# Kernel tuning notes

Measured on AMD Instinct MI355X. Metric: run time of the kernel, lower is better.

## Reference

```python
import jax, jax.numpy as jnp
import numpy as np

B, S, D = 2, 2048, 768
H, DK, DV = 12, 64, 64


def setup_inputs() -> dict:
    key = jax.random.key(0)
    ks = jax.random.split(key, 12)
    sc = 0.02
    return {
        'q': jax.random.normal(ks[0], (B, S, D), jnp.float32),
        'k': jax.random.normal(ks[1], (B, S, D), jnp.float32),
        'v': jax.random.normal(ks[2], (B, S, D), jnp.float32),
        'mask': jnp.zeros((B, H, S, S), jnp.float32),
        'Wq': jax.random.normal(ks[3], (D, H * DK), jnp.float32) * sc,
        'bq': jnp.zeros((H * DK,), jnp.float32),
        'Wk': jax.random.normal(ks[4], (D, H * DK), jnp.float32) * sc,
        'bk': jnp.zeros((H * DK,), jnp.float32),
        'Wv': jax.random.normal(ks[5], (D, H * DV), jnp.float32) * sc,
        'bv': jnp.zeros((H * DV,), jnp.float32),
        'Wo': jax.random.normal(ks[6], (H * DV, D), jnp.float32) * sc,
        'bo': jnp.zeros((D,), jnp.float32),
    }


def reference(q, k, v, mask, Wq, bq, Wk, bk, Wv, bv, Wo, bo):
    b, s, _ = q.shape
    # projections -> [B, H, S, Dk/Dv]
    Q = (q @ Wq + bq).reshape(b, s, H, DK).transpose(0, 2, 1, 3)
    K = (k @ Wk + bk).reshape(b, s, H, DK).transpose(0, 2, 1, 3)
    V = (v @ Wv + bv).reshape(b, s, H, DV).transpose(0, 2, 1, 3)
    scale = 1.0 / np.sqrt(DK).astype(np.float32)
    scores = jnp.einsum('bhqd,bhkd->bhqk', Q, K) * scale + mask
    attn = jax.nn.softmax(scores, axis=-1)  # dropout rate 0.0 -> identity
    ctx = jnp.einsum('bhqk,bhkd->bhqd', attn, V)
    ctx = ctx.transpose(0, 2, 1, 3).reshape(b, s, H * DV)
    out = ctx @ Wo + bo
    return out, attn
```

## Files before the change

### kernel.cpp

```cpp
#include <hip/hip_runtime.h>
#include <hip/hip_bf16.h>

typedef unsigned short u16;
typedef __attribute__((ext_vector_type(8))) short s16x8;
typedef __attribute__((ext_vector_type(4))) float f32x4;

#define MFMA16(a, b, c) __builtin_amdgcn_mfma_f32_16x16x32_bf16((a), (b), (c), 0, 0, 0)

__device__ __forceinline__ float b2f(u16 u) {
    union { float f; unsigned int i; } c; c.i = ((unsigned int)u) << 16; return c.f;
}
__device__ __forceinline__ u16 f2b(float f) {
    union { float f; unsigned int i; } c; c.f = f;
    unsigned int i = c.i;
    return (u16)((i + 0x7fffu + ((i >> 16) & 1u)) >> 16);
}

__device__ __forceinline__ s16x8 load8b(const void* base, size_t idx, int isf32) {
    if (!isf32) {
        return *(const s16x8*)((const u16*)base + idx);
    } else {
        const float* p = (const float*)base + idx;
        f32x4 a = *(const f32x4*)p;
        f32x4 b = *(const f32x4*)(p + 4);
        s16x8 v;
        v[0] = (short)f2b(a[0]); v[1] = (short)f2b(a[1]);
        v[2] = (short)f2b(a[2]); v[3] = (short)f2b(a[3]);
        v[4] = (short)f2b(b[0]); v[5] = (short)f2b(b[1]);
        v[6] = (short)f2b(b[2]); v[7] = (short)f2b(b[3]);
        return v;
    }
}
__device__ __forceinline__ float loadsc(const void* base, size_t idx, int isf32) {
    return isf32 ? ((const float*)base)[idx] : b2f(((const u16*)base)[idx]);
}
__device__ __forceinline__ float loadsc_nt(const void* base, size_t idx, int isf32) {
    if (isf32) return __builtin_nontemporal_load((const float*)base + idx);
    u16 u = __builtin_nontemporal_load((const u16*)base + idx);
    return b2f(u);
}

__global__ __launch_bounds__(64) void k_detect(const u16* __restrict__ q, int* __restrict__ flag) {
    int t = threadIdx.x;
    int cnt = 0;
#pragma unroll
    for (int i = 0; i < 16; i++) {
        u16 u = q[t * 16 + i];
        int e = (u >> 7) & 0xFF;
        cnt += (e >= 110 && e <= 135) ? 1 : 0;
    }
#pragma unroll
    for (int off = 32; off > 0; off >>= 1) cnt += __shfl_down(cnt, off);
    if (t == 0) *flag = (cnt < 850) ? 1 : 0;
}

__global__ __launch_bounds__(256) void k_transpose(
    const void* __restrict__ w0, const void* __restrict__ w1,
    const void* __restrict__ w2, const void* __restrict__ w3,
    u16* __restrict__ wt, const int* __restrict__ flag)
{
    __shared__ __align__(16) u16 T[64 * 65];
    const int isf32 = *flag;
    const int z = blockIdx.z;
    const void* W = (z == 0) ? w0 : (z == 1) ? w1 : (z == 2) ? w2 : w3;
    u16* WT = wt + (size_t)z * 589824;
    const int n0 = blockIdx.x * 64, k0 = blockIdx.y * 64;
    const int t = threadIdx.x;
    const int r = t >> 3, c = (t & 7) * 8;
    for (int rr = r; rr < 64; rr += 32) {
        s16x8 v = load8b(W, (size_t)(k0 + rr) * 768 + n0 + c, isf32);
#pragma unroll
        for (int j = 0; j < 8; j++) T[(c + j) * 65 + rr] = (u16)v[j];
    }
    __syncthreads();
    const int n = t >> 3, kc = (t & 7) * 8;
    for (int nn = n; nn < 64; nn += 32) {
        s16x8 v;
#pragma unroll
        for (int j = 0; j < 8; j++) v[j] = (short)T[nn * 65 + kc + j];
        *(s16x8*)&WT[(size_t)(n0 + nn) * 768 + k0 + kc] = v;
    }
}

__device__ __forceinline__ void gemm_body(
    const void* __restrict__ A, int a_isf32, const u16* __restrict__ WT,
    const void* __restrict__ bias, int b_isf32, void* __restrict__ out,
    int out_isf32, int epi, int head, int m0)
{
    __shared__ __align__(16) u16 As[128 * 72];
    __shared__ __align__(16) u16 Bs[64 * 72];
    const int t = threadIdx.x;
    const int lane = t & 63, wave = t >> 6;
    const int quad = lane >> 4, l16 = lane & 15;
    const int mrow_base = (wave >> 1) * 64;
    const int ncol_base = (wave & 1) * 32;
    const int hbase = head * 64;

    f32x4 acc[4][2];
#pragma unroll
    for (int mt = 0; mt < 4; mt++)
#pragma unroll
        for (int nt = 0; nt < 2; nt++) acc[mt][nt] = (f32x4){0.f, 0.f, 0.f, 0.f};

    for (int k0 = 0; k0 < 768; k0 += 64) {
#pragma unroll
        for (int i = 0; i < 4; i++) {
            int seg = t + 256 * i;
            int r = seg >> 3, c = (seg & 7) * 8;
            *(s16x8*)&As[r * 72 + c] = load8b(A, (size_t)(m0 + r) * 768 + k0 + c, a_isf32);
        }
#pragma unroll
        for (int i = 0; i < 2; i++) {
            int seg = t + 256 * i;
            int r = seg >> 3, c = (seg & 7) * 8;
            *(s16x8*)&Bs[r * 72 + c] = *(const s16x8*)&WT[(size_t)(hbase + r) * 768 + k0 + c];
        }
        __syncthreads();
#pragma unroll
        for (int ks = 0; ks < 2; ks++) {
            s16x8 af[4], bf[2];
#pragma unroll
            for (int mt = 0; mt < 4; mt++)
                af[mt] = *(const s16x8*)&As[(mrow_base + mt * 16 + l16) * 72 + ks * 32 + quad * 8];
#pragma unroll
            for (int nt = 0; nt < 2; nt++)
                bf[nt] = *(const s16x8*)&Bs[(ncol_base + nt * 16 + l16) * 72 + ks * 32 + quad * 8];
#pragma unroll
            for (int mt = 0; mt < 4; mt++)
#pragma unroll
                for (int nt = 0; nt < 2; nt++)
                    acc[mt][nt] = MFMA16(af[mt], bf[nt], acc[mt][nt]);
        }
        __syncthreads();
    }

    if (epi == 2) {
#pragma unroll
        for (int mt = 0; mt < 4; mt++)
#pragma unroll
            for (int nt = 0; nt < 2; nt++) {
                int nc = ncol_base + nt * 16 + l16;
                float bvv = loadsc(bias, hbase + nc, b_isf32);
#pragma unroll
                for (int r = 0; r < 4; r++) {
                    int m = m0 + mrow_base + mt * 16 + quad * 4 + r;
                    float val = acc[mt][nt][r] + bvv;
                    size_t idx = (size_t)m * 768 + hbase + nc;
                    if (out_isf32) ((float*)out)[idx] = val;
                    else           ((u16*)out)[idx] = f2b(val);
                }
            }
    } else if (epi == 0) {
        u16* ob = (u16*)out;
#pragma unroll
        for (int mt = 0; mt < 4; mt++)
#pragma unroll
            for (int nt = 0; nt < 2; nt++) {
                int nc = ncol_base + nt * 16 + l16;
                float bvv = loadsc(bias, hbase + nc, b_isf32);
#pragma unroll
                for (int r = 0; r < 4; r++) {
                    int m = m0 + mrow_base + mt * 16 + quad * 4 + r;
                    int bidx = m >> 11, s = m & 2047;
                    ob[(((size_t)bidx * 12 + head) * 2048 + s) * 64 + nc] =
                        f2b(acc[mt][nt][r] + bvv);
                }
            }
    } else {
        u16* ob = (u16*)out;
        u16* Ts = As;
#pragma unroll
        for (int mt = 0; mt < 4; mt++)
#pragma unroll
            for (int nt = 0; nt < 2; nt++) {
                int nc = ncol_base + nt * 16 + l16;
                float bvv = loadsc(bias, hbase + nc, b_isf32);
#pragma unroll
                for (int r = 0; r < 4; r++) {
                    int ml = mrow_base + mt * 16 + quad * 4 + r;
                    Ts[nc * 136 + ml] = f2b(acc[mt][nt][r] + bvv);
                }
            }
        __syncthreads();
        const int bidx = m0 >> 11, sbase = m0 & 2047;
#pragma unroll
        for (int i = 0; i < 4; i++) {
            int seg = t + 256 * i;
            int dv = seg >> 4, scc = (seg & 15) * 8;
            s16x8 vv = *(const s16x8*)&Ts[dv * 136 + scc];
            *(s16x8*)&ob[(((size_t)bidx * 12 + head) * 64 + dv) * 2048 + sbase + scc] = vv;
        }
    }
}

__global__ __launch_bounds__(256) void k_qkv(
    const void* __restrict__ q, const void* __restrict__ k, const void* __restrict__ v,
    const u16* __restrict__ wt,
    const void* __restrict__ bq, const void* __restrict__ bk, const void* __restrict__ bv,
    u16* __restrict__ Q, u16* __restrict__ K, u16* __restrict__ Vt,
    const int* __restrict__ flag)
{
    const int isf32 = *flag;
    const int z = blockIdx.z;
    const void* A = (z == 0) ? q : (z == 1) ? k : v;
    const u16* WTz = wt + (size_t)z * 589824;
    const void* bias = (z == 0) ? bq : (z == 1) ? bk : bv;
    u16* out = (z == 0) ? Q : (z == 1) ? K : Vt;
    gemm_body(A, isf32, WTz, bias, isf32, out, 0, (z == 2) ? 1 : 0, blockIdx.y, blockIdx.x * 128);
}

__global__ __launch_bounds__(256) void k_oproj(
    const u16* __restrict__ ctx, const u16* __restrict__ wto,
    const void* __restrict__ bo, void* __restrict__ out,
    const int* __restrict__ flag)
{
    const int isf32 = *flag;
    gemm_body(ctx, 0, wto, bo, isf32, out, isf32, 2, blockIdx.y, blockIdx.x * 128);
}

__device__ __forceinline__ int sw_off(int row, int col) {
    int unit = col >> 3;
    int slot = (unit + row) & 7;
    return row * 2048 + (((unit & ~7) | slot) << 3) + (col & 7);
}

__global__ __launch_bounds__(512, 4) void k_attn(
    const u16* __restrict__ Q, const u16* __restrict__ K,
    const u16* __restrict__ Vt, const void* __restrict__ mask,
    void* __restrict__ outbase, u16* __restrict__ ctx,
    const int* __restrict__ flag)
{
    __shared__ __align__(16) u16 sc[16 * 2048];
    __shared__ __align__(16) float part[1024];
    __shared__ float wmax[16][8];
    const int isf32 = *flag;
    const int t = threadIdx.x;
    const int lane = t & 63, wave = t >> 6;
    const int quad = lane >> 4, l16 = lane & 15;
    const int q0 = blockIdx.x * 16;
    const int h = blockIdx.y, b = blockIdx.z;
    const int bh = b * 12 + h;

    const u16* Qb = Q + ((size_t)bh * 2048 + q0) * 64;
    const s16x8 qf0 = *(const s16x8*)&Qb[l16 * 64 + quad * 8];
    const s16x8 qf1 = *(const s16x8*)&Qb[l16 * 64 + 32 + quad * 8];

    const u16* Kb = K + (size_t)bh * 2048 * 64;
    const size_t mrow0 = ((size_t)bh * 2048 + q0) * 2048;

    float rm[4] = {-3.4e38f, -3.4e38f, -3.4e38f, -3.4e38f};
#pragma unroll 4
    for (int it = 0; it < 16; it++) {
        const int kc = it * 128 + wave * 16;
        const u16* kp = &Kb[(size_t)(kc + l16) * 64 + quad * 8];
        s16x8 kf0 = *(const s16x8*)kp;
        s16x8 kf1 = *(const s16x8*)(kp + 32);
        f32x4 a = (f32x4){0.f, 0.f, 0.f, 0.f};
        a = MFMA16(qf0, kf0, a);
        a = MFMA16(qf1, kf1, a);
        const int col = kc + l16;
#pragma unroll
        for (int r = 0; r < 4; r++) {
            const int row = quad * 4 + r;
            float m = loadsc_nt(mask, mrow0 + (size_t)row * 2048 + col, isf32);
            float x = a[r] * 0.125f + m;
            sc[sw_off(row, col)] = f2b(x);
            rm[r] = fmaxf(rm[r], x);
        }
    }
#pragma unroll
    for (int off = 8; off > 0; off >>= 1)
#pragma unroll
        for (int r = 0; r < 4; r++) rm[r] = fmaxf(rm[r], __shfl_xor(rm[r], off));
    if (l16 == 0) {
#pragma unroll
        for (int r = 0; r < 4; r++) wmax[quad * 4 + r][wave] = rm[r];
    }
    __syncthreads();

    const int row = t >> 5, j32 = t & 31;
    float mx = wmax[row][0];
#pragma unroll
    for (int w = 1; w < 8; w++) mx = fmaxf(mx, wmax[row][w]);

    float sum = 0.f;
#pragma unroll 4
    for (int i = 0; i < 8; i++) {
        const int c0 = j32 * 8 + i * 256;
        s16x8* sp = (s16x8*)&sc[sw_off(row, c0)];
        s16x8 sv = *sp, nv;
#pragma unroll
        for (int j = 0; j < 8; j++) {
            float e = __expf(b2f((u16)sv[j]) - mx);
            nv[j] = (short)f2b(e);
            sum += e;
        }
        *sp = nv;
    }
#pragma unroll
    for (int off = 16; off > 0; off >>= 1) sum += __shfl_xor(sum, off);
    const float inv = 1.0f / sum;

    const size_t aoff = 3145728 + mrow0 + (size_t)row * 2048;
#pragma unroll 2
    for (int i = 0; i < 8; i++) {
        const int c0 = j32 * 8 + i * 256;
        s16x8* sp = (s16x8*)&sc[sw_off(row, c0)];
        s16x8 sv = *sp, pv;
        float p[8];
#pragma unroll
        for (int j = 0; j < 8; j++) {
            p[j] = b2f((u16)sv[j]) * inv;
            pv[j] = (short)f2b(p[j]);
        }
        *sp = pv;
        if (isf32) {
            float* arow = (float*)outbase + aoff;
            f32x4 lo = (f32x4){p[0], p[1], p[2], p[3]};
            f32x4 hi = (f32x4){p[4], p[5], p[6], p[7]};
            __builtin_nontemporal_store(lo, (f32x4*)&arow[c0]);
            __builtin_nontemporal_store(hi, (f32x4*)&arow[c0 + 4]);
        } else {
            u16* arow = (u16*)outbase + aoff;
            __builtin_nontemporal_store(pv, (s16x8*)&arow[c0]);
        }
    }
    __syncthreads();

    const int wg = wave >> 2;
    const int dv = (wave & 3) * 16 + l16;
    const u16* vrow = Vt + ((size_t)bh * 64 + dv) * 2048;
    f32x4 o = (f32x4){0.f, 0.f, 0.f, 0.f};
    const int kbase = wg * 32;
#pragma unroll 4
    for (int kk = 0; kk < 32; kk++) {
        const int kcol = (kbase + kk) * 32 + quad * 8;
        s16x8 pa = *(const s16x8*)&sc[sw_off(l16, kcol)];
        s16x8 vb = *(const s16x8*)&vrow[kcol];
        o = MFMA16(pa, vb, o);
    }
    if (wg == 1) *(f32x4*)&part[((wave & 3) * 64 + lane) * 4] = o;
    __syncthreads();
    if (wg == 0) {
        f32x4 o2 = *(const f32x4*)&part[((wave & 3) * 64 + lane) * 4];
#pragma unroll
        for (int r = 0; r < 4; r++)
            ctx[((size_t)b * 2048 + q0 + quad * 4 + r) * 768 + h * 64 + dv] =
                f2b(o[r] + o2[r]);
    }
}

extern "C" void kernel_launch(void* const* d_in, const int* in_sizes, int n_in,
                              void* d_out, int out_size, void* d_ws, size_t ws_size,
                              hipStream_t stream) {
    const void* q    = d_in[0];
    const void* k    = d_in[1];
    const void* v    = d_in[2];
    const void* mask = d_in[3];
    const void* Wq   = d_in[4];
    const void* bq   = d_in[5];
    const void* Wk   = d_in[6];
    const void* bk   = d_in[7];
    const void* Wv   = d_in[8];
    const void* bv   = d_in[9];
    const void* Wo   = d_in[10];
    const void* bo   = d_in[11];

    u16* ws  = (u16*)d_ws;
    u16* WT  = ws;
    u16* Qb  = ws + 2359296;
    u16* Kb  = ws + 5505024;
    u16* Vtb = ws + 8650752;
    u16* ctx = ws + 11796480;
    int* flag = (int*)(ws + 14942208);

    k_detect<<<1, 64, 0, stream>>>((const u16*)q, flag);
    k_transpose<<<dim3(12, 12, 4), 256, 0, stream>>>(Wq, Wk, Wv, Wo, WT, flag);
    k_qkv<<<dim3(32, 12, 3), 256, 0, stream>>>(q, k, v, WT, bq, bk, bv, Qb, Kb, Vtb, flag);
    k_attn<<<dim3(128, 12, 2), 512, 0, stream>>>(Qb, Kb, Vtb, mask, d_out, ctx, flag);
    k_oproj<<<dim3(32, 12, 1), 256, 0, stream>>>(ctx, WT + 3 * 589824, bo, d_out, flag);
}
```

Before: 1.008 ms.

## Vectorize mask loads in softmax pass and defer normalization to PV output

Result: faster. 924.3 us (-8.3%).

```diff
diff --git a/kernel.cpp b/kernel.cpp
--- a/kernel.cpp
+++ b/kernel.cpp
@@ -34,10 +34,18 @@
 __device__ __forceinline__ float loadsc(const void* base, size_t idx, int isf32) {
     return isf32 ? ((const float*)base)[idx] : b2f(((const u16*)base)[idx]);
 }
-__device__ __forceinline__ float loadsc_nt(const void* base, size_t idx, int isf32) {
-    if (isf32) return __builtin_nontemporal_load((const float*)base + idx);
-    u16 u = __builtin_nontemporal_load((const u16*)base + idx);
-    return b2f(u);
+__device__ __forceinline__ void load8f_nt(const void* base, size_t idx, int isf32, float* o) {
+    if (!isf32) {
+        s16x8 m = __builtin_nontemporal_load((const s16x8*)((const u16*)base + idx));
+#pragma unroll
+        for (int j = 0; j < 8; j++) o[j] = b2f((u16)m[j]);
+    } else {
+        const float* p = (const float*)base + idx;
+        f32x4 a = __builtin_nontemporal_load((const f32x4*)p);
+        f32x4 b = __builtin_nontemporal_load((const f32x4*)(p + 4));
+        o[0] = a[0]; o[1] = a[1]; o[2] = a[2]; o[3] = a[3];
+        o[4] = b[0]; o[5] = b[1]; o[6] = b[2]; o[7] = b[3];
+    }
 }
 
 __global__ __launch_bounds__(64) void k_detect(const u16* __restrict__ q, int* __restrict__ flag) {
@@ -232,7 +240,7 @@
 {
     __shared__ __align__(16) u16 sc[16 * 2048];
     __shared__ __align__(16) float part[1024];
-    __shared__ float wmax[16][8];
+    __shared__ float invs[16];
     const int isf32 = *flag;
     const int t = threadIdx.x;
     const int lane = t & 63, wave = t >> 6;
@@ -248,7 +256,6 @@
     const u16* Kb = K + (size_t)bh * 2048 * 64;
     const size_t mrow0 = ((size_t)bh * 2048 + q0) * 2048;
 
-    float rm[4] = {-3.4e38f, -3.4e38f, -3.4e38f, -3.4e38f};
 #pragma unroll 4
     for (int it = 0; it < 16; it++) {
         const int kc = it * 128 + wave * 16;
@@ -260,28 +267,30 @@
         a = MFMA16(qf1, kf1, a);
         const int col = kc + l16;
 #pragma unroll
-        for (int r = 0; r < 4; r++) {
-            const int row = quad * 4 + r;
-            float m = loadsc_nt(mask, mrow0 + (size_t)row * 2048 + col, isf32);
-            float x = a[r] * 0.125f + m;
-            sc[sw_off(row, col)] = f2b(x);
-            rm[r] = fmaxf(rm[r], x);
-        }
-    }
-#pragma unroll
-    for (int off = 8; off > 0; off >>= 1)
-#pragma unroll
-        for (int r = 0; r < 4; r++) rm[r] = fmaxf(rm[r], __shfl_xor(rm[r], off));
-    if (l16 == 0) {
-#pragma unroll
-        for (int r = 0; r < 4; r++) wmax[quad * 4 + r][wave] = rm[r];
+        for (int r = 0; r < 4; r++)
+            sc[sw_off(quad * 4 + r, col)] = f2b(a[r] * 0.125f);
     }
     __syncthreads();
 
     const int row = t >> 5, j32 = t & 31;
-    float mx = wmax[row][0];
-#pragma unroll
-    for (int w = 1; w < 8; w++) mx = fmaxf(mx, wmax[row][w]);
+    float mx = -3.4e38f;
+#pragma unroll 4
+    for (int i = 0; i < 8; i++) {
+        const int c0 = j32 * 8 + i * 256;
+        float mk[8];
+        load8f_nt(mask, mrow0 + (size_t)row * 2048 + c0, isf32, mk);
+        s16x8* sp = (s16x8*)&sc[sw_off(row, c0)];
+        s16x8 sv = *sp, nv;
+#pragma unroll
+        for (int j = 0; j < 8; j++) {
+            float x = b2f((u16)sv[j]) + mk[j];
+            nv[j] = (short)f2b(x);
+            mx = fmaxf(mx, x);
+        }
+        *sp = nv;
+    }
+#pragma unroll
+    for (int off = 16; off > 0; off >>= 1) mx = fmaxf(mx, __shfl_xor(mx, off));
 
     float sum = 0.f;
 #pragma unroll 4
@@ -300,29 +309,28 @@
 #pragma unroll
     for (int off = 16; off > 0; off >>= 1) sum += __shfl_xor(sum, off);
     const float inv = 1.0f / sum;
+    if (j32 == 0) invs[row] = inv;
 
     const size_t aoff = 3145728 + mrow0 + (size_t)row * 2048;
 #pragma unroll 2
     for (int i = 0; i < 8; i++) {
         const int c0 = j32 * 8 + i * 256;
-        s16x8* sp = (s16x8*)&sc[sw_off(row, c0)];
-        s16x8 sv = *sp, pv;
-        float p[8];
-#pragma unroll
-        for (int j = 0; j < 8; j++) {
-            p[j] = b2f((u16)sv[j]) * inv;
-            pv[j] = (short)f2b(p[j]);
-        }
-        *sp = pv;
+        s16x8 sv = *(const s16x8*)&sc[sw_off(row, c0)];
         if (isf32) {
             float* arow = (float*)outbase + aoff;
-            f32x4 lo = (f32x4){p[0], p[1], p[2], p[3]};
-            f32x4 hi = (f32x4){p[4], p[5], p[6], p[7]};
-            __builtin_nontemporal_store(lo, (f32x4*)&arow[c0]);
-            __builtin_nontemporal_store(hi, (f32x4*)&arow[c0 + 4]);
+            f32x4 lo, hi;
+#pragma unroll
+            for (int j = 0; j < 4; j++) lo[j] = b2f((u16)sv[j]) * inv;
+#pragma unroll
+            for (int j = 0; j < 4; j++) hi[j] = b2f((u16)sv[j + 4]) * inv;
+            *(f32x4*)&arow[c0] = lo;
+            *(f32x4*)&arow[c0 + 4] = hi;
         } else {
             u16* arow = (u16*)outbase + aoff;
-            __builtin_nontemporal_store(pv, (s16x8*)&arow[c0]);
+            s16x8 pv;
+#pragma unroll
+            for (int j = 0; j < 8; j++) pv[j] = (short)f2b(b2f((u16)sv[j]) * inv);
+            *(s16x8*)&arow[c0] = pv;
         }
     }
     __syncthreads();
@@ -344,9 +352,10 @@
     if (wg == 0) {
         f32x4 o2 = *(const f32x4*)&part[((wave & 3) * 64 + lane) * 4];
 #pragma unroll
-        for (int r = 0; r < 4; r++)
-            ctx[((size_t)b * 2048 + q0 + quad * 4 + r) * 768 + h * 64 + dv] =
-                f2b(o[r] + o2[r]);
+        for (int r = 0; r < 4; r++) {
+            float val = (o[r] + o2[r]) * invs[quad * 4 + r];
+            ctx[((size_t)b * 2048 + q0 + quad * 4 + r) * 768 + h * 64 + dv] = f2b(val);
+        }
     }
 }
 
```
